# Kernel tuning notes

Hardware: AMD Instinct MI355X
Metric: run time of the kernel (lower is better)

The kernel has to match this reference:

```python
import jax, jax.numpy as jnp
import numpy as np

N_HEAD = 8
EPS = 1e-08


def setup_inputs() -> dict:
    key = jax.random.key(0)
    ks = jax.random.split(key, 4)
    B, T, C = 2, 2048, 512
    x = jax.random.normal(ks[0], (B, T, C), dtype=jnp.float32)
    attention_mask = jnp.ones((B, T, T), dtype=jnp.float32)  # causal structure irrelevant: only diagonal used
    c_attn_kernel = jax.random.normal(ks[1], (C, 3 * C), dtype=jnp.float32) * 0.02
    c_attn_bias = jnp.zeros((3 * C,), dtype=jnp.float32)
    c_proj_kernel = jax.random.normal(ks[2], (C, C), dtype=jnp.float32) * (0.02 / np.sqrt(2 * 12))
    c_proj_bias = jnp.zeros((C,), dtype=jnp.float32)
    return {
        "x": x,
        "attention_mask": attention_mask,
        "c_attn_kernel": c_attn_kernel,
        "c_attn_bias": c_attn_bias,
        "c_proj_kernel": c_proj_kernel,
        "c_proj_bias": c_proj_bias,
    }


def reference(x, attention_mask, c_attn_kernel, c_attn_bias, c_proj_kernel, c_proj_bias):
    B, T, C = x.shape
    H = N_HEAD
    D = C // H

    qkv = x @ c_attn_kernel + c_attn_bias            # (B,T,3C)
    q, k, v = jnp.split(qkv, 3, axis=2)

    # (B,T,C) -> (B,H,T,D)
    def to_heads(t):
        return t.reshape(B, T, H, D).transpose(0, 2, 1, 3)

    q, k, v = to_heads(q), to_heads(k), to_heads(v)

    phi_q = jax.nn.elu(q) + 1.0
    phi_k = jax.nn.elu(k) + 1.0

    valid_positions = jnp.diagonal(attention_mask, axis1=1, axis2=2)  # (B,T)
    position_mask = valid_positions[:, None, :, None]                 # (B,1,T,1)
    phi_k = phi_k * position_mask
    v = v * position_mask

    # (B,H,T,D,D) outer products, cumulative over time (memory-bound hot spot)
    kv_outer = jnp.einsum('bhti,bhtj->bhtij', phi_k, v)
    kv_cumsum = jnp.cumsum(kv_outer, axis=2)
    k_cumsum = jnp.cumsum(phi_k, axis=2)

    numerator = jnp.einsum('bhti,bhtij->bhtj', phi_q, kv_cumsum)      # (B,H,T,D)
    denominator = jnp.einsum('bhti,bhti->bht', phi_q, k_cumsum)       # (B,H,T)
    denominator = jnp.maximum(denominator, EPS)

    y = numerator / denominator[..., None]
    y = y.transpose(0, 2, 1, 3).reshape(B, T, C)
    y = y @ c_proj_kernel + c_proj_bias
    return y
```

## Files before the change

kernel.cpp:

```cpp
#include <hip/hip_runtime.h>
#include <math.h>

using short8 = __attribute__((ext_vector_type(8))) short;
using f32x4  = __attribute__((ext_vector_type(4))) float;
typedef unsigned short ushort_t;

#define MFMA16(a,b,c) __builtin_amdgcn_mfma_f32_16x16x32_bf16((a),(b),(c),0,0,0)

#define BB 2
#define TT 2048
#define CC 512
#define HH 8
#define DD 64
#define N3 1536
#define NCH 32

__device__ __forceinline__ float bf2f(ushort_t u){ unsigned int x=((unsigned int)u)<<16; return __builtin_bit_cast(float,x); }
__device__ __forceinline__ ushort_t f2bf(float f){ unsigned int u=__builtin_bit_cast(unsigned int,f); u += 0x7FFFu + ((u>>16)&1u); return (ushort_t)(u>>16); }
__device__ __forceinline__ float elu1(float v){ return v > 0.f ? v + 1.f : expf(v); }

__global__ void prep(const float* __restrict__ x, const float* __restrict__ amask,
                     const float* __restrict__ W, const float* __restrict__ Pw,
                     ushort_t* __restrict__ xb, ushort_t* __restrict__ wt,
                     ushort_t* __restrict__ pt, float* __restrict__ mdiag)
{
  int gid = blockIdx.x * blockDim.x + threadIdx.x;
  int gsz = gridDim.x * blockDim.x;
  for (int i = gid; i < BB*TT*CC; i += gsz) xb[i] = f2bf(x[i]);
  for (int i = gid; i < CC*N3; i += gsz) { int k = i / N3, n = i - k*N3; wt[n*CC + k] = f2bf(W[i]); }
  for (int i = gid; i < CC*CC; i += gsz) { int k = i >> 9, n = i & 511; pt[n*CC + k] = f2bf(Pw[i]); }
  for (int i = gid; i < BB*TT; i += gsz) { int b = i >> 11, t = i & 2047; mdiag[i] = amask[((size_t)b*TT + t)*TT + t]; }
}

__global__ __launch_bounds__(256) void gemm_qkv(const ushort_t* __restrict__ A, const ushort_t* __restrict__ Bt,
    const float* __restrict__ bias, const float* __restrict__ mdiag,
    ushort_t* __restrict__ phiQ, ushort_t* __restrict__ phiK, ushort_t* __restrict__ vB)
{
  __shared__ __align__(16) ushort_t lA[128][40];
  __shared__ __align__(16) ushort_t lB[128][40];
  const int tid = threadIdx.x;
  const int lane = tid & 63, wid = tid >> 6;
  const int g = lane >> 4, lr = lane & 15;
  const int bm = blockIdx.y * 128, bn = blockIdx.x * 128;
  const int wm = (wid >> 1) * 64, wn = (wid & 1) * 64;
  f32x4 acc[4][4] = {};
  for (int k0 = 0; k0 < CC; k0 += 32) {
    #pragma unroll
    for (int it = 0; it < 2; ++it) {
      int flat = tid + it * 256;
      int row = flat >> 2, seg = flat & 3;
      *(short8*)&lA[row][seg*8] = *(const short8*)&A[(size_t)(bm+row)*CC + k0 + seg*8];
      *(short8*)&lB[row][seg*8] = *(const short8*)&Bt[(size_t)(bn+row)*CC + k0 + seg*8];
    }
    __syncthreads();
    short8 af[4], bf[4];
    #pragma unroll
    for (int mf=0;mf<4;++mf) af[mf] = *(const short8*)&lA[wm+mf*16+lr][g*8];
    #pragma unroll
    for (int nf=0;nf<4;++nf) bf[nf] = *(const short8*)&lB[wn+nf*16+lr][g*8];
    #pragma unroll
    for (int mf=0;mf<4;++mf)
      #pragma unroll
      for (int nf=0;nf<4;++nf)
        acc[mf][nf] = MFMA16(af[mf], bf[nf], acc[mf][nf]);
    __syncthreads();
  }
  #pragma unroll
  for (int mf=0;mf<4;++mf) {
    int m0 = bm + wm + mf*16 + g*4;
    #pragma unroll
    for (int nf=0;nf<4;++nf) {
      int n = bn + wn + nf*16 + lr;
      int which = n >> 9, h = (n >> 6) & 7, d = n & 63;
      #pragma unroll
      for (int r=0;r<4;++r) {
        int mm = m0 + r;
        int b = mm >> 11, t = mm & 2047;
        float v = acc[mf][nf][r] + bias[n];
        size_t oidx = (((size_t)(b*HH + h))*TT + t)*DD + d;
        if (which == 0)       phiQ[oidx] = f2bf(elu1(v));
        else if (which == 1)  phiK[oidx] = f2bf(elu1(v) * mdiag[mm]);
        else                  vB[oidx]   = f2bf(v * mdiag[mm]);
      }
    }
  }
}

__global__ __launch_bounds__(64) void chunk_state(const ushort_t* __restrict__ phiK,
                                                  const ushort_t* __restrict__ vB,
                                                  float* __restrict__ sChunk)
{
  int bid = blockIdx.x;
  int bh = bid >> 5, c = bid & 31;
  int lane = threadIdx.x;
  int g = lane >> 4, lr = lane & 15;
  __shared__ __align__(16) ushort_t KT[64][72];
  __shared__ __align__(16) ushort_t VT[80][72];
  int t0 = c * 64;
  const ushort_t* kptr = &phiK[((size_t)bh*TT + t0 + lane)*DD];
  const ushort_t* vptr = &vB  [((size_t)bh*TT + t0 + lane)*DD];
  #pragma unroll
  for (int j8 = 0; j8 < 8; ++j8) {
    short8 kk = *(const short8*)&kptr[j8*8];
    short8 vv = *(const short8*)&vptr[j8*8];
    #pragma unroll
    for (int jj=0; jj<8; ++jj) { KT[j8*8+jj][lane] = (ushort_t)kk[jj]; VT[j8*8+jj][lane] = (ushort_t)vv[jj]; }
  }
  VT[64][lane] = 0x3F80;
  #pragma unroll
  for (int j=65; j<80; ++j) VT[j][lane] = 0;
  __syncthreads();
  float* dst = &sChunk[(size_t)bid * (80*64)];
  #pragma unroll
  for (int mf=0; mf<4; ++mf)
    for (int nf=0; nf<5; ++nf) {
      f32x4 acc = {0.f,0.f,0.f,0.f};
      #pragma unroll
      for (int kf=0; kf<2; ++kf) {
        short8 a = *(const short8*)&KT[mf*16+lr][kf*32 + g*8];
        short8 b = *(const short8*)&VT[nf*16+lr][kf*32 + g*8];
        acc = MFMA16(a, b, acc);
      }
      *(f32x4*)&dst[(size_t)(nf*16+lr)*64 + mf*16 + g*4] = acc;
    }
}

__global__ void scan_states(const float* __restrict__ sChunk, ushort_t* __restrict__ sPrev)
{
  int bx = blockIdx.x;
  int bh = bx / 20, seg = bx % 20;
  int e = seg*256 + threadIdx.x;
  size_t base = (size_t)bh*NCH*5120 + e;
  float run = 0.f;
  for (int c = 0; c < NCH; ++c) {
    sPrev[base + (size_t)c*5120] = f2bf(run);
    run += sChunk[base + (size_t)c*5120];
  }
}

__global__ __launch_bounds__(64) void chunk_out(const ushort_t* __restrict__ phiQ,
    const ushort_t* __restrict__ phiK, const ushort_t* __restrict__ vB,
    const ushort_t* __restrict__ sPrev, ushort_t* __restrict__ ya)
{
  int bid = blockIdx.x;
  int bh = bid >> 5, c = bid & 31;
  int lane = threadIdx.x, g = lane >> 4, lr = lane & 15;
  __shared__ __align__(16) ushort_t P[64][72];
  __shared__ __align__(16) ushort_t VT[64][72];
  __shared__ float den[64];
  int t0 = c * 64;
  size_t qbase = (size_t)bh*TT + t0;
  short8 qf[4][2];
  #pragma unroll
  for (int mf=0;mf<4;++mf)
    #pragma unroll
    for (int kf=0;kf<2;++kf)
      qf[mf][kf] = *(const short8*)&phiQ[(qbase + mf*16 + lr)*DD + kf*32 + g*8];
  f32x4 accs[4][4] = {};
  #pragma unroll
  for (int nf=0;nf<4;++nf)
    #pragma unroll
    for (int kf=0;kf<2;++kf) {
      short8 bk = *(const short8*)&phiK[(qbase + nf*16 + lr)*DD + kf*32 + g*8];
      #pragma unroll
      for (int mf=0;mf<4;++mf) accs[mf][nf] = MFMA16(qf[mf][kf], bk, accs[mf][nf]);
    }
  f32x4 accn[4][5] = {};
  size_t sbase = (size_t)bid * 5120;
  #pragma unroll
  for (int nf=0;nf<5;++nf)
    #pragma unroll
    for (int kf=0;kf<2;++kf) {
      short8 bs = *(const short8*)&sPrev[sbase + (size_t)(nf*16+lr)*64 + kf*32 + g*8];
      #pragma unroll
      for (int mf=0;mf<4;++mf) accn[mf][nf] = MFMA16(qf[mf][kf], bs, accn[mf][nf]);
    }
  {
    const ushort_t* vptr = &vB[(qbase + lane)*DD];
    #pragma unroll
    for (int j8=0;j8<8;++j8) {
      short8 vv = *(const short8*)&vptr[j8*8];
      #pragma unroll
      for (int jj=0;jj<8;++jj) VT[j8*8+jj][lane] = (ushort_t)vv[jj];
    }
  }
  #pragma unroll
  for (int mf=0;mf<4;++mf)
    #pragma unroll
    for (int nf=0;nf<4;++nf)
      #pragma unroll
      for (int r=0;r<4;++r) {
        int t = mf*16 + g*4 + r, s = nf*16 + lr;
        P[t][s] = f2bf((s <= t) ? accs[mf][nf][r] : 0.f);
      }
  __syncthreads();
  if (lr == 0)
    #pragma unroll
    for (int mf=0;mf<4;++mf)
      #pragma unroll
      for (int r=0;r<4;++r) den[mf*16 + g*4 + r] = accn[mf][4][r];
  __syncthreads();
  {
    float di = den[lane];
    for (int s=0;s<64;++s) di += bf2f(P[lane][s]);
    di = fmaxf(di, 1e-8f);
    den[lane] = 1.0f / di;
  }
  __syncthreads();
  short8 pf[4][2];
  #pragma unroll
  for (int mf=0;mf<4;++mf)
    #pragma unroll
    for (int kf=0;kf<2;++kf)
      pf[mf][kf] = *(const short8*)&P[mf*16+lr][kf*32 + g*8];
  #pragma unroll
  for (int nf=0;nf<4;++nf)
    #pragma unroll
    for (int kf=0;kf<2;++kf) {
      short8 vf = *(const short8*)&VT[nf*16+lr][kf*32 + g*8];
      #pragma unroll
      for (int mf=0;mf<4;++mf) accn[mf][nf] = MFMA16(pf[mf][kf], vf, accn[mf][nf]);
    }
  int b = bh >> 3, h = bh & 7;
  #pragma unroll
  for (int mf=0;mf<4;++mf) {
    float inv[4];
    #pragma unroll
    for (int r=0;r<4;++r) inv[r] = den[mf*16 + g*4 + r];
    #pragma unroll
    for (int nf=0;nf<4;++nf)
      #pragma unroll
      for (int r=0;r<4;++r) {
        int t = t0 + mf*16 + g*4 + r;
        int col = h*64 + nf*16 + lr;
        ya[((size_t)b*TT + t)*CC + col] = f2bf(accn[mf][nf][r] * inv[r]);
      }
  }
}

__global__ __launch_bounds__(256) void gemm_proj(const ushort_t* __restrict__ A, const ushort_t* __restrict__ Bt,
                                                 const float* __restrict__ bias, float* __restrict__ out)
{
  __shared__ __align__(16) ushort_t lA[128][40];
  __shared__ __align__(16) ushort_t lB[128][40];
  const int tid = threadIdx.x;
  const int lane = tid & 63, wid = tid >> 6;
  const int g = lane >> 4, lr = lane & 15;
  const int bm = blockIdx.y * 128, bn = blockIdx.x * 128;
  const int wm = (wid >> 1) * 64, wn = (wid & 1) * 64;
  f32x4 acc[4][4] = {};
  for (int k0 = 0; k0 < CC; k0 += 32) {
    #pragma unroll
    for (int it = 0; it < 2; ++it) {
      int flat = tid + it * 256;
      int row = flat >> 2, seg = flat & 3;
      *(short8*)&lA[row][seg*8] = *(const short8*)&A[(size_t)(bm+row)*CC + k0 + seg*8];
      *(short8*)&lB[row][seg*8] = *(const short8*)&Bt[(size_t)(bn+row)*CC + k0 + seg*8];
    }
    __syncthreads();
    short8 af[4], bf[4];
    #pragma unroll
    for (int mf=0;mf<4;++mf) af[mf] = *(const short8*)&lA[wm+mf*16+lr][g*8];
    #pragma unroll
    for (int nf=0;nf<4;++nf) bf[nf] = *(const short8*)&lB[wn+nf*16+lr][g*8];
    #pragma unroll
    for (int mf=0;mf<4;++mf)
      #pragma unroll
      for (int nf=0;nf<4;++nf)
        acc[mf][nf] = MFMA16(af[mf], bf[nf], acc[mf][nf]);
    __syncthreads();
  }
  #pragma unroll
  for (int mf=0;mf<4;++mf) {
    int m0 = bm + wm + mf*16 + g*4;
    #pragma unroll
    for (int nf=0;nf<4;++nf) {
      int n = bn + wn + nf*16 + lr;
      #pragma unroll
      for (int r=0;r<4;++r)
        out[(size_t)(m0 + r)*CC + n] = acc[mf][nf][r] + bias[n];
    }
  }
}

extern "C" void kernel_launch(void* const* d_in, const int* in_sizes, int n_in,
                              void* d_out, int out_size, void* d_ws, size_t ws_size,
                              hipStream_t stream)
{
  const float* x     = (const float*)d_in[0];
  const float* amask = (const float*)d_in[1];
  const float* wqkv  = (const float*)d_in[2];
  const float* bqkv  = (const float*)d_in[3];
  const float* wproj = (const float*)d_in[4];
  const float* bproj = (const float*)d_in[5];
  float* out = (float*)d_out;
  char* ws = (char*)d_ws;

  ushort_t* xb    = (ushort_t*)(ws + 0);
  ushort_t* wt    = (ushort_t*)(ws + 4194304);
  ushort_t* pt    = (ushort_t*)(ws + 5767168);
  float*    mdiag = (float*)   (ws + 6291456);
  ushort_t* phiQ  = (ushort_t*)(ws + 6307840);
  ushort_t* phiK  = (ushort_t*)(ws + 10502144);
  ushort_t* vB    = (ushort_t*)(ws + 14696448);
  ushort_t* ya    = (ushort_t*)(ws + 18890752);
  float*    sChunk= (float*)   (ws + 23085056);
  ushort_t* sPrev = (ushort_t*)(ws + 33570816);

  prep<<<dim3(1024), dim3(256), 0, stream>>>(x, amask, wqkv, wproj, xb, wt, pt, mdiag);
  gemm_qkv<<<dim3(12,32), dim3(256), 0, stream>>>(xb, wt, bqkv, mdiag, phiQ, phiK, vB);
  chunk_state<<<dim3(512), dim3(64), 0, stream>>>(phiK, vB, sChunk);
  scan_states<<<dim3(16*20), dim3(256), 0, stream>>>(sChunk, sPrev);
  chunk_out<<<dim3(512), dim3(64), 0, stream>>>(phiQ, phiK, vB, sPrev, ya);
  gemm_proj<<<dim3(4,32), dim3(256), 0, stream>>>(ya, pt, bproj, out);
}
```

Measured before the change: 154.9 us.

## Write transposed K/V from QKV GEMM, tile prep transposes, vectorize scan, pack chunk kernels

The QKV GEMM epilogue now also writes phiK and V in a time-contiguous transposed layout. This lets chunk_state and chunk_out load MFMA fragments straight from global memory instead of transposing through LDS. The prep kernel uses shared-memory tiled transposes for the weights and vectorized bf16 conversion for x. The scan uses float4 loads with prefetch. Chunk kernels pack four chunks per 256-thread block, and the denominator now comes from an extra MFMA against a ones column, spread with a shuffle. The cost is extra uncoalesced transposed global stores in the GEMM epilogue and more workspace.

```diff
diff --git a/kernel.cpp b/kernel.cpp
--- a/kernel.cpp
+++ b/kernel.cpp
@@ -3,6 +3,7 @@
 
 using short8 = __attribute__((ext_vector_type(8))) short;
 using f32x4  = __attribute__((ext_vector_type(4))) float;
+using us4    = __attribute__((ext_vector_type(4))) unsigned short;
 typedef unsigned short ushort_t;
 
 #define MFMA16(a,b,c) __builtin_amdgcn_mfma_f32_16x16x32_bf16((a),(b),(c),0,0,0)
@@ -19,22 +20,46 @@
 __device__ __forceinline__ ushort_t f2bf(float f){ unsigned int u=__builtin_bit_cast(unsigned int,f); u += 0x7FFFu + ((u>>16)&1u); return (ushort_t)(u>>16); }
 __device__ __forceinline__ float elu1(float v){ return v > 0.f ? v + 1.f : expf(v); }
 
-__global__ void prep(const float* __restrict__ x, const float* __restrict__ amask,
+__global__ __launch_bounds__(256) void prep(const float* __restrict__ x, const float* __restrict__ amask,
                      const float* __restrict__ W, const float* __restrict__ Pw,
                      ushort_t* __restrict__ xb, ushort_t* __restrict__ wt,
                      ushort_t* __restrict__ pt, float* __restrict__ mdiag)
 {
-  int gid = blockIdx.x * blockDim.x + threadIdx.x;
-  int gsz = gridDim.x * blockDim.x;
-  for (int i = gid; i < BB*TT*CC; i += gsz) xb[i] = f2bf(x[i]);
-  for (int i = gid; i < CC*N3; i += gsz) { int k = i / N3, n = i - k*N3; wt[n*CC + k] = f2bf(W[i]); }
-  for (int i = gid; i < CC*CC; i += gsz) { int k = i >> 9, n = i & 511; pt[n*CC + k] = f2bf(Pw[i]); }
-  for (int i = gid; i < BB*TT; i += gsz) { int b = i >> 11, t = i & 2047; mdiag[i] = amask[((size_t)b*TT + t)*TT + t]; }
+  __shared__ float tile[32][33];
+  int bid = blockIdx.x, tid = threadIdx.x;
+  int tx = tid & 31, ty0 = tid >> 5;
+  if (bid < 768) {
+    int nt = bid % 48, kt = bid / 48;
+    #pragma unroll
+    for (int i=0;i<4;++i){ int ty=ty0+8*i; tile[ty][tx] = W[(size_t)(kt*32+ty)*N3 + nt*32+tx]; }
+    __syncthreads();
+    #pragma unroll
+    for (int i=0;i<4;++i){ int ty=ty0+8*i; wt[(size_t)(nt*32+ty)*CC + kt*32+tx] = f2bf(tile[tx][ty]); }
+  } else if (bid < 1024) {
+    int tt = bid - 768; int nt = tt & 15, kt = tt >> 4;
+    #pragma unroll
+    for (int i=0;i<4;++i){ int ty=ty0+8*i; tile[ty][tx] = Pw[(size_t)(kt*32+ty)*CC + nt*32+tx]; }
+    __syncthreads();
+    #pragma unroll
+    for (int i=0;i<4;++i){ int ty=ty0+8*i; pt[(size_t)(nt*32+ty)*CC + kt*32+tx] = f2bf(tile[tx][ty]); }
+  } else if (bid < 1056) {
+    int g = (bid-1024)*256 + tid;
+    const f32x4* xs = (const f32x4*)x;
+    us4* xo = (us4*)xb;
+    for (int i=g; i<(BB*TT*CC)/4; i+=32*256) {
+      f32x4 v = xs[i];
+      us4 o = { f2bf(v[0]), f2bf(v[1]), f2bf(v[2]), f2bf(v[3]) };
+      xo[i] = o;
+    }
+  } else {
+    for (int i=tid; i<BB*TT; i+=256) { int b=i>>11, t=i&2047; mdiag[i]=amask[((size_t)b*TT+t)*TT+t]; }
+  }
 }
 
 __global__ __launch_bounds__(256) void gemm_qkv(const ushort_t* __restrict__ A, const ushort_t* __restrict__ Bt,
     const float* __restrict__ bias, const float* __restrict__ mdiag,
-    ushort_t* __restrict__ phiQ, ushort_t* __restrict__ phiK, ushort_t* __restrict__ vB)
+    ushort_t* __restrict__ phiQ, ushort_t* __restrict__ phiK,
+    ushort_t* __restrict__ kT, ushort_t* __restrict__ vT)
 {
   __shared__ __align__(16) ushort_t lA[128][40];
   __shared__ __align__(16) ushort_t lB[128][40];
@@ -77,77 +102,82 @@
         int mm = m0 + r;
         int b = mm >> 11, t = mm & 2047;
         float v = acc[mf][nf][r] + bias[n];
-        size_t oidx = (((size_t)(b*HH + h))*TT + t)*DD + d;
+        size_t bh = (size_t)(b*HH + h);
+        size_t oidx = (bh*TT + t)*DD + d;
         if (which == 0)       phiQ[oidx] = f2bf(elu1(v));
-        else if (which == 1)  phiK[oidx] = f2bf(elu1(v) * mdiag[mm]);
-        else                  vB[oidx]   = f2bf(v * mdiag[mm]);
+        else if (which == 1)  { ushort_t e = f2bf(elu1(v) * mdiag[mm]); phiK[oidx] = e; kT[(bh*DD + d)*TT + t] = e; }
+        else                  vT[(bh*DD + d)*TT + t] = f2bf(v * mdiag[mm]);
       }
     }
   }
 }
 
-__global__ __launch_bounds__(64) void chunk_state(const ushort_t* __restrict__ phiK,
-                                                  const ushort_t* __restrict__ vB,
-                                                  float* __restrict__ sChunk)
-{
-  int bid = blockIdx.x;
-  int bh = bid >> 5, c = bid & 31;
-  int lane = threadIdx.x;
-  int g = lane >> 4, lr = lane & 15;
-  __shared__ __align__(16) ushort_t KT[64][72];
-  __shared__ __align__(16) ushort_t VT[80][72];
+__global__ __launch_bounds__(256) void chunk_state(const ushort_t* __restrict__ kT,
+                                                   const ushort_t* __restrict__ vT,
+                                                   float* __restrict__ sChunk)
+{
+  int wid = threadIdx.x >> 6;
+  int cid = blockIdx.x * 4 + wid;
+  int bh = cid >> 5, c = cid & 31;
+  int lane = threadIdx.x & 63, g = lane >> 4, lr = lane & 15;
   int t0 = c * 64;
-  const ushort_t* kptr = &phiK[((size_t)bh*TT + t0 + lane)*DD];
-  const ushort_t* vptr = &vB  [((size_t)bh*TT + t0 + lane)*DD];
-  #pragma unroll
-  for (int j8 = 0; j8 < 8; ++j8) {
-    short8 kk = *(const short8*)&kptr[j8*8];
-    short8 vv = *(const short8*)&vptr[j8*8];
-    #pragma unroll
-    for (int jj=0; jj<8; ++jj) { KT[j8*8+jj][lane] = (ushort_t)kk[jj]; VT[j8*8+jj][lane] = (ushort_t)vv[jj]; }
-  }
-  VT[64][lane] = 0x3F80;
-  #pragma unroll
-  for (int j=65; j<80; ++j) VT[j][lane] = 0;
-  __syncthreads();
-  float* dst = &sChunk[(size_t)bid * (80*64)];
-  #pragma unroll
-  for (int mf=0; mf<4; ++mf)
-    for (int nf=0; nf<5; ++nf) {
+  short8 af[4][2];
+  #pragma unroll
+  for (int mf=0;mf<4;++mf)
+    #pragma unroll
+    for (int kf=0;kf<2;++kf)
+      af[mf][kf] = *(const short8*)&kT[((size_t)bh*DD + mf*16+lr)*TT + t0 + kf*32 + g*8];
+  short8 onesf;
+  {
+    short ov = (lr == 0) ? (short)0x3F80 : (short)0;
+    #pragma unroll
+    for (int j=0;j<8;++j) onesf[j] = ov;
+  }
+  float* dst = &sChunk[(size_t)cid * 5120];
+  #pragma unroll
+  for (int nf=0;nf<5;++nf) {
+    short8 bfr[2];
+    #pragma unroll
+    for (int kf=0;kf<2;++kf)
+      bfr[kf] = (nf < 4) ? *(const short8*)&vT[((size_t)bh*DD + nf*16+lr)*TT + t0 + kf*32 + g*8]
+                         : onesf;
+    #pragma unroll
+    for (int mf=0;mf<4;++mf) {
       f32x4 acc = {0.f,0.f,0.f,0.f};
       #pragma unroll
-      for (int kf=0; kf<2; ++kf) {
-        short8 a = *(const short8*)&KT[mf*16+lr][kf*32 + g*8];
-        short8 b = *(const short8*)&VT[nf*16+lr][kf*32 + g*8];
-        acc = MFMA16(a, b, acc);
-      }
+      for (int kf=0;kf<2;++kf) acc = MFMA16(af[mf][kf], bfr[kf], acc);
       *(f32x4*)&dst[(size_t)(nf*16+lr)*64 + mf*16 + g*4] = acc;
     }
-}
-
-__global__ void scan_states(const float* __restrict__ sChunk, ushort_t* __restrict__ sPrev)
+  }
+}
+
+__global__ __launch_bounds__(256) void scan_states(const float* __restrict__ sChunk, ushort_t* __restrict__ sPrev)
 {
   int bx = blockIdx.x;
-  int bh = bx / 20, seg = bx % 20;
-  int e = seg*256 + threadIdx.x;
-  size_t base = (size_t)bh*NCH*5120 + e;
-  float run = 0.f;
+  int bh = bx / 5, seg = bx % 5;
+  int e4 = seg*256 + threadIdx.x;
+  const f32x4* src = (const f32x4*)(sChunk + (size_t)bh*NCH*5120) + e4;
+  us4* dst = (us4*)(sPrev + (size_t)bh*NCH*5120) + e4;
+  f32x4 run = {0.f,0.f,0.f,0.f};
+  f32x4 nxt = src[0];
   for (int c = 0; c < NCH; ++c) {
-    sPrev[base + (size_t)c*5120] = f2bf(run);
-    run += sChunk[base + (size_t)c*5120];
-  }
-}
-
-__global__ __launch_bounds__(64) void chunk_out(const ushort_t* __restrict__ phiQ,
-    const ushort_t* __restrict__ phiK, const ushort_t* __restrict__ vB,
+    f32x4 cur = nxt;
+    if (c+1 < NCH) nxt = src[(size_t)(c+1)*1280];
+    us4 o = { f2bf(run[0]), f2bf(run[1]), f2bf(run[2]), f2bf(run[3]) };
+    dst[(size_t)c*1280] = o;
+    run += cur;
+  }
+}
+
+__global__ __launch_bounds__(256) void chunk_out(const ushort_t* __restrict__ phiQ,
+    const ushort_t* __restrict__ phiK, const ushort_t* __restrict__ vT,
     const ushort_t* __restrict__ sPrev, ushort_t* __restrict__ ya)
 {
-  int bid = blockIdx.x;
-  int bh = bid >> 5, c = bid & 31;
-  int lane = threadIdx.x, g = lane >> 4, lr = lane & 15;
-  __shared__ __align__(16) ushort_t P[64][72];
-  __shared__ __align__(16) ushort_t VT[64][72];
-  __shared__ float den[64];
+  __shared__ __align__(16) ushort_t P[4][64][72];
+  int wid = threadIdx.x >> 6;
+  int cid = blockIdx.x * 4 + wid;
+  int bh = cid >> 5, c = cid & 31;
+  int lane = threadIdx.x & 63, g = lane >> 4, lr = lane & 15;
   int t0 = c * 64;
   size_t qbase = (size_t)bh*TT + t0;
   short8 qf[4][2];
@@ -166,7 +196,7 @@
       for (int mf=0;mf<4;++mf) accs[mf][nf] = MFMA16(qf[mf][kf], bk, accs[mf][nf]);
     }
   f32x4 accn[4][5] = {};
-  size_t sbase = (size_t)bid * 5120;
+  size_t sbase = (size_t)cid * 5120;
   #pragma unroll
   for (int nf=0;nf<5;++nf)
     #pragma unroll
@@ -175,15 +205,6 @@
       #pragma unroll
       for (int mf=0;mf<4;++mf) accn[mf][nf] = MFMA16(qf[mf][kf], bs, accn[mf][nf]);
     }
-  {
-    const ushort_t* vptr = &vB[(qbase + lane)*DD];
-    #pragma unroll
-    for (int j8=0;j8<8;++j8) {
-      short8 vv = *(const short8*)&vptr[j8*8];
-      #pragma unroll
-      for (int jj=0;jj<8;++jj) VT[j8*8+jj][lane] = (ushort_t)vv[jj];
-    }
-  }
   #pragma unroll
   for (int mf=0;mf<4;++mf)
     #pragma unroll
@@ -191,51 +212,49 @@
       #pragma unroll
       for (int r=0;r<4;++r) {
         int t = mf*16 + g*4 + r, s = nf*16 + lr;
-        P[t][s] = f2bf((s <= t) ? accs[mf][nf][r] : 0.f);
+        P[wid][t][s] = f2bf((s <= t) ? accs[mf][nf][r] : 0.f);
       }
   __syncthreads();
-  if (lr == 0)
-    #pragma unroll
-    for (int mf=0;mf<4;++mf)
-      #pragma unroll
-      for (int r=0;r<4;++r) den[mf*16 + g*4 + r] = accn[mf][4][r];
-  __syncthreads();
+  short8 pf[4][2];
+  #pragma unroll
+  for (int mf=0;mf<4;++mf)
+    #pragma unroll
+    for (int kf=0;kf<2;++kf)
+      pf[mf][kf] = *(const short8*)&P[wid][mf*16+lr][kf*32 + g*8];
+  short8 onesf;
   {
-    float di = den[lane];
-    for (int s=0;s<64;++s) di += bf2f(P[lane][s]);
-    di = fmaxf(di, 1e-8f);
-    den[lane] = 1.0f / di;
-  }
-  __syncthreads();
-  short8 pf[4][2];
-  #pragma unroll
-  for (int mf=0;mf<4;++mf)
-    #pragma unroll
-    for (int kf=0;kf<2;++kf)
-      pf[mf][kf] = *(const short8*)&P[mf*16+lr][kf*32 + g*8];
-  #pragma unroll
-  for (int nf=0;nf<4;++nf)
+    short ov = (lr == 0) ? (short)0x3F80 : (short)0;
+    #pragma unroll
+    for (int j=0;j<8;++j) onesf[j] = ov;
+  }
+  #pragma unroll
+  for (int nf=0;nf<5;++nf)
     #pragma unroll
     for (int kf=0;kf<2;++kf) {
-      short8 vf = *(const short8*)&VT[nf*16+lr][kf*32 + g*8];
+      short8 vf = (nf < 4) ? *(const short8*)&vT[((size_t)bh*DD + nf*16+lr)*TT + t0 + kf*32 + g*8]
+                           : onesf;
       #pragma unroll
       for (int mf=0;mf<4;++mf) accn[mf][nf] = MFMA16(pf[mf][kf], vf, accn[mf][nf]);
     }
+  float invb[4][4];
+  #pragma unroll
+  for (int mf=0;mf<4;++mf)
+    #pragma unroll
+    for (int r=0;r<4;++r) {
+      float iv = 1.0f / fmaxf(accn[mf][4][r], 1e-8f);
+      invb[mf][r] = __shfl(iv, lane & 48);
+    }
   int b = bh >> 3, h = bh & 7;
   #pragma unroll
-  for (int mf=0;mf<4;++mf) {
-    float inv[4];
-    #pragma unroll
-    for (int r=0;r<4;++r) inv[r] = den[mf*16 + g*4 + r];
+  for (int mf=0;mf<4;++mf)
     #pragma unroll
     for (int nf=0;nf<4;++nf)
       #pragma unroll
       for (int r=0;r<4;++r) {
         int t = t0 + mf*16 + g*4 + r;
         int col = h*64 + nf*16 + lr;
-        ya[((size_t)b*TT + t)*CC + col] = f2bf(accn[mf][nf][r] * inv[r]);
+        ya[((size_t)b*TT + t)*CC + col] = f2bf(accn[mf][nf][r] * invb[mf][r]);
       }
-  }
 }
 
 __global__ __launch_bounds__(256) void gemm_proj(const ushort_t* __restrict__ A, const ushort_t* __restrict__ Bt,
@@ -302,15 +321,16 @@
   float*    mdiag = (float*)   (ws + 6291456);
   ushort_t* phiQ  = (ushort_t*)(ws + 6307840);
   ushort_t* phiK  = (ushort_t*)(ws + 10502144);
-  ushort_t* vB    = (ushort_t*)(ws + 14696448);
-  ushort_t* ya    = (ushort_t*)(ws + 18890752);
-  float*    sChunk= (float*)   (ws + 23085056);
-  ushort_t* sPrev = (ushort_t*)(ws + 33570816);
-
-  prep<<<dim3(1024), dim3(256), 0, stream>>>(x, amask, wqkv, wproj, xb, wt, pt, mdiag);
-  gemm_qkv<<<dim3(12,32), dim3(256), 0, stream>>>(xb, wt, bqkv, mdiag, phiQ, phiK, vB);
-  chunk_state<<<dim3(512), dim3(64), 0, stream>>>(phiK, vB, sChunk);
-  scan_states<<<dim3(16*20), dim3(256), 0, stream>>>(sChunk, sPrev);
-  chunk_out<<<dim3(512), dim3(64), 0, stream>>>(phiQ, phiK, vB, sPrev, ya);
+  ushort_t* kT    = (ushort_t*)(ws + 14696448);
+  ushort_t* vT    = (ushort_t*)(ws + 18890752);
+  ushort_t* ya    = (ushort_t*)(ws + 23085056);
+  float*    sChunk= (float*)   (ws + 27279360);
+  ushort_t* sPrev = (ushort_t*)(ws + 37765120);
+
+  prep<<<dim3(1057), dim3(256), 0, stream>>>(x, amask, wqkv, wproj, xb, wt, pt, mdiag);
+  gemm_qkv<<<dim3(12,32), dim3(256), 0, stream>>>(xb, wt, bqkv, mdiag, phiQ, phiK, kT, vT);
+  chunk_state<<<dim3(128), dim3(256), 0, stream>>>(kT, vT, sChunk);
+  scan_states<<<dim3(80), dim3(256), 0, stream>>>(sChunk, sPrev);
+  chunk_out<<<dim3(128), dim3(256), 0, stream>>>(phiQ, phiK, vT, sPrev, ya);
   gemm_proj<<<dim3(4,32), dim3(256), 0, stream>>>(ya, pt, bproj, out);
 }
```

Result: slower. 195.2 us (+26.0%).
